# Optimization experiments

Hardware: AMD Instinct MI355X
Metric: run time of the kernel (lower is better)

The kernel has to match this reference:

```python
import jax, jax.numpy as jnp
import numpy as np

BETA = 0.9
ADAPT_RATE = 0.1


def _surrogate_spike(x):
    gate = jax.nn.sigmoid(5.0 * x)
    hard = (x > 0).astype(x.dtype)
    return jax.lax.stop_gradient(hard - gate) + gate


def setup_inputs() -> dict:
    key = jax.random.key(0)
    k1, k2, k3, k4, k5 = jax.random.split(key, 5)
    B, T, D, H = 64, 256, 512, 1024
    x = jax.random.normal(k1, (B, T, D), dtype=jnp.float32)
    # fc_in: Linear(D, H); fc_out: Linear(H, 1)
    W_in = jax.random.normal(k2, (H, D), dtype=jnp.float32) * (1.0 / np.sqrt(D))
    b_in = jax.random.normal(k3, (H,), dtype=jnp.float32) * 0.01
    W_out = jax.random.normal(k4, (1, H), dtype=jnp.float32) * (1.0 / np.sqrt(H))
    b_out = jax.random.normal(k5, (1,), dtype=jnp.float32) * 0.01
    return {"x": x, "W_in": W_in, "b_in": b_in, "W_out": W_out, "b_out": b_out}


def reference(x, W_in, b_in, W_out, b_out):
    B, T, D = x.shape
    H = W_in.shape[0]
    # batch fc_in over all timesteps outside the recurrence
    pre = jnp.einsum('btd,hd->bth', x, W_in) + b_in  # [B,T,H]

    def step(carry, p_t):
        mem, adapt = carry
        mem = BETA * mem + p_t - adapt
        spk = _surrogate_spike(mem)
        adapt = adapt + ADAPT_RATE * spk
        mem = mem - spk  # reset_mode == 'subtract'
        return (mem, adapt), spk

    init = (jnp.zeros((B, H), x.dtype), jnp.zeros((B, H), x.dtype))
    _, spks = jax.lax.scan(step, init, jnp.swapaxes(pre, 0, 1))  # spks: [T,B,H]

    # mean_t fc_out(spk_t) == fc_out(mean_t spk_t) since fc_out is affine
    spk_mean = spks.mean(axis=0)  # [B,H]
    return spk_mean @ W_out.T + b_out  # [B,1]
```

## Files before the change

### kernel.cpp

```cpp
#include <hip/hip_runtime.h>

constexpr int Bb = 64;
constexpr int Tt = 256;
constexpr int Dd = 512;
constexpr int Hh = 1024;
constexpr int Mm = Bb * Tt;

typedef _Float16 half8 __attribute__((ext_vector_type(8)));
typedef _Float16 half4v __attribute__((ext_vector_type(4)));
typedef float floatx16 __attribute__((ext_vector_type(16)));

#define GPTR(x) ((const __attribute__((address_space(1))) void*)(x))
#define LPTR(x) ((__attribute__((address_space(3))) void*)(x))

__global__ __launch_bounds__(256) void convert_t(const float* __restrict__ x,
                                                 const float* __restrict__ Win,
                                                 _Float16* __restrict__ xh,
                                                 _Float16* __restrict__ xl,
                                                 _Float16* __restrict__ wh,
                                                 _Float16* __restrict__ wl,
                                                 const float* __restrict__ bout,
                                                 float* __restrict__ out) {
    __shared__ _Float16 lh[64 * 72];
    __shared__ _Float16 ll[64 * 72];
    const int tid = threadIdx.x;
    const int k0 = blockIdx.x * 64;

    if (blockIdx.x == 0 && blockIdx.y == 0 && tid < Bb) out[tid] = bout[0];

    const float* src;
    _Float16 *dh, *dl;
    int nrows, m0;
    if (blockIdx.y < 256) {
        src = x; dh = xh; dl = xl; nrows = Mm; m0 = blockIdx.y * 64;
    } else {
        src = Win; dh = wh; dl = wl; nrows = Hh; m0 = (blockIdx.y - 256) * 64;
    }

#pragma unroll
    for (int i = 0; i < 4; ++i) {
        const int lin = tid + i * 256;
        const int row = lin >> 4;
        const int c4 = (lin & 15) * 4;
        const float4 v = *(const float4*)(src + (size_t)(m0 + row) * Dd + k0 + c4);
        const float va[4] = {v.x, v.y, v.z, v.w};
        half4v h, l;
#pragma unroll
        for (int q = 0; q < 4; ++q) {
            const _Float16 hi = (_Float16)va[q];
            h[q] = hi;
            l[q] = (_Float16)((va[q] - (float)hi) * 4096.0f);
        }
        *(half4v*)&lh[row * 72 + c4] = h;
        *(half4v*)&ll[row * 72 + c4] = l;
    }
    __syncthreads();
#pragma unroll
    for (int i = 0; i < 2; ++i) {
        const int lin = tid + i * 256;
        const int kc = lin >> 6;
        const int mm = lin & 63;
        const half8 h = *(const half8*)&lh[mm * 72 + kc * 8];
        const half8 l = *(const half8*)&ll[mm * 72 + kc * 8];
        const size_t g = (size_t)(k0 / 8 + kc) * nrows + m0 + mm;
        *(half8*)(dh + g * 8) = h;
        *(half8*)(dl + g * 8) = l;
    }
}

__global__ __launch_bounds__(256, 2) void gemm_fused(const _Float16* __restrict__ xh,
                                                     const _Float16* __restrict__ xl,
                                                     const _Float16* __restrict__ wh,
                                                     const _Float16* __restrict__ wl,
                                                     const float* __restrict__ bin,
                                                     const float* __restrict__ Wout,
                                                     float* __restrict__ out) {
    __shared__ _Float16 ldsA[2][2][8192];

    const int tid = threadIdx.x;
    const int id = blockIdx.x;
    const int j  = id & 7;
    const int q  = id >> 3;
    const int nt = q & 15;
    const int b  = (q >> 4) * 8 + j;
    const int m0 = b * Tt;
    const int n0 = nt * 64;

    const int lane = tid & 63;
    const int wave = tid >> 6;
    const int lr = lane & 31;
    const int lk = lane >> 5;

    floatx16 acc[2][2], accx[2][2];
#pragma unroll
    for (int mi = 0; mi < 2; ++mi)
#pragma unroll
        for (int ni = 0; ni < 2; ++ni)
#pragma unroll
            for (int r = 0; r < 16; ++r) { acc[mi][ni][r] = 0.0f; accx[mi][ni][r] = 0.0f; }

#define STAGE_A(buf, kc0)                                                            \
    do {                                                                             \
        _Pragma("unroll")                                                            \
        for (int i_ = 0; i_ < 4; ++i_) {                                             \
            const int c_ = tid + i_ * 256;                                           \
            const int kp_ = c_ >> 8;                                                 \
            const int row_ = c_ & 255;                                               \
            const size_t ga_ = ((size_t)((kc0) + kp_) * Mm + m0 + row_) * 8;         \
            __builtin_amdgcn_global_load_lds(GPTR(xh + ga_), LPTR(&ldsA[buf][0][c_ * 8]), 16, 0, 0); \
            __builtin_amdgcn_global_load_lds(GPTR(xl + ga_), LPTR(&ldsA[buf][1][c_ * 8]), 16, 0, 0); \
        }                                                                            \
    } while (0)

    const size_t bbase = (size_t)(n0 + lr) * 8;
    half8 bset[2][4];
#define LOAD_B(rot, hs)                                                              \
    do {                                                                             \
        const size_t off_ = (size_t)((hs) * 2 + lk) * (Hh * 8) + bbase;              \
        bset[rot][0] = *(const half8*)(wh + off_);                                   \
        bset[rot][1] = *(const half8*)(wh + off_ + 256);                             \
        bset[rot][2] = *(const half8*)(wl + off_);                                   \
        bset[rot][3] = *(const half8*)(wl + off_ + 256);                             \
    } while (0)

    STAGE_A(0, 0);
    LOAD_B(0, 0);

    for (int ss = 0; ss < 16; ++ss) {
        __syncthreads();
        if (ss < 15) STAGE_A((ss + 1) & 1, (ss + 1) * 4);
        const int cur = ss & 1;
#pragma unroll
        for (int s2 = 0; s2 < 2; ++s2) {
            const int hs = ss * 2 + s2;
            const int rot = hs & 1;
            if (hs < 31) LOAD_B(rot ^ 1, hs + 1);

            half8 ah[2], al[2];
#pragma unroll
            for (int mi = 0; mi < 2; ++mi) {
                const int ci = (s2 * 2 + lk) * 256 + wave * 64 + mi * 32 + lr;
                ah[mi] = *(const half8*)&ldsA[cur][0][ci * 8];
                al[mi] = *(const half8*)&ldsA[cur][1][ci * 8];
            }
#pragma unroll
            for (int mi = 0; mi < 2; ++mi)
#pragma unroll
                for (int ni = 0; ni < 2; ++ni) {
                    acc[mi][ni]  = __builtin_amdgcn_mfma_f32_32x32x16_f16(ah[mi], bset[rot][ni],     acc[mi][ni], 0, 0, 0);
                    accx[mi][ni] = __builtin_amdgcn_mfma_f32_32x32x16_f16(ah[mi], bset[rot][2 + ni], accx[mi][ni], 0, 0, 0);
                    accx[mi][ni] = __builtin_amdgcn_mfma_f32_32x32x16_f16(al[mi], bset[rot][ni],     accx[mi][ni], 0, 0, 0);
                }
        }
    }
#undef STAGE_A
#undef LOAD_B

    __syncthreads();
    float* scanbuf = (float*)ldsA;

#pragma unroll
    for (int p = 0; p < 2; ++p) {
        const float bv = bin[n0 + p * 32 + lr];
#pragma unroll
        for (int mi = 0; mi < 2; ++mi)
#pragma unroll
            for (int r = 0; r < 16; ++r) {
                const int row = (r & 3) + 8 * (r >> 2) + 4 * lk;
                const int t = wave * 64 + mi * 32 + row;
                scanbuf[p * 8192 + t * 32 + lr] =
                    acc[mi][p][r] + accx[mi][p][r] * (1.0f / 4096.0f) + bv;
            }
    }
    __syncthreads();

    if (wave == 0) {
        const float* sb = scanbuf + (lane >> 5) * 8192 + (lane & 31);
        float mem = 0.0f, adapt = 0.0f, cnt = 0.0f;
#pragma unroll 8
        for (int t = 0; t < Tt; ++t) {
            const float v = sb[t * 32];
            mem = 0.9f * mem + v - adapt;
            const float spk = (mem > 0.0f) ? 1.0f : 0.0f;
            adapt += 0.1f * spk;
            mem -= spk;
            cnt += spk;
        }
        float val = cnt * Wout[n0 + lane] * (1.0f / (float)Tt);
#pragma unroll
        for (int off = 32; off > 0; off >>= 1) val += __shfl_down(val, off, 64);
        if (lane == 0) atomicAdd(&out[b], val);
    }
}

#define BK 16
#define BMP 132
__global__ __launch_bounds__(256) void gemm_pre(const float* __restrict__ x,
                                                const float* __restrict__ Win,
                                                const float* __restrict__ bin,
                                                float* __restrict__ pre) {
    __shared__ float As[BK][BMP];
    __shared__ float Bs[BK][BMP];
    const int tid = threadIdx.x;
    const int m0 = blockIdx.y * 128;
    const int n0 = blockIdx.x * 128;
    const int tx = tid & 15;
    const int ty = tid >> 4;
    float acc[8][8];
#pragma unroll
    for (int i = 0; i < 8; ++i)
#pragma unroll
        for (int jj = 0; jj < 8; ++jj) acc[i][jj] = 0.0f;
    const float* Aptr = x + (size_t)m0 * Dd;
    const float* Bptr = Win + (size_t)n0 * Dd;
    for (int k0 = 0; k0 < Dd; k0 += BK) {
#pragma unroll
        for (int i = 0; i < 2; ++i) {
            const int lin = tid + i * 256;
            const int row = lin >> 2;
            const int kq = (lin & 3) << 2;
            const float4 av = *(const float4*)(Aptr + (size_t)row * Dd + k0 + kq);
            const float4 bv = *(const float4*)(Bptr + (size_t)row * Dd + k0 + kq);
            As[kq + 0][row] = av.x; As[kq + 1][row] = av.y;
            As[kq + 2][row] = av.z; As[kq + 3][row] = av.w;
            Bs[kq + 0][row] = bv.x; Bs[kq + 1][row] = bv.y;
            Bs[kq + 2][row] = bv.z; Bs[kq + 3][row] = bv.w;
        }
        __syncthreads();
#pragma unroll
        for (int kk = 0; kk < BK; ++kk) {
            const float4 a0 = *(const float4*)&As[kk][ty * 4];
            const float4 a1 = *(const float4*)&As[kk][ty * 4 + 64];
            const float4 b0 = *(const float4*)&Bs[kk][tx * 4];
            const float4 b1 = *(const float4*)&Bs[kk][tx * 4 + 64];
            const float a[8] = {a0.x, a0.y, a0.z, a0.w, a1.x, a1.y, a1.z, a1.w};
            const float b[8] = {b0.x, b0.y, b0.z, b0.w, b1.x, b1.y, b1.z, b1.w};
#pragma unroll
            for (int i = 0; i < 8; ++i)
#pragma unroll
                for (int jj = 0; jj < 8; ++jj) acc[i][jj] += a[i] * b[jj];
        }
        __syncthreads();
    }
#pragma unroll
    for (int i = 0; i < 8; ++i) {
        const int m = m0 + ((i < 4) ? (ty * 4 + i) : (64 + ty * 4 + i - 4));
#pragma unroll
        for (int half = 0; half < 2; ++half) {
            const int n = n0 + tx * 4 + half * 64;
            float4 v;
            v.x = acc[i][half * 4 + 0] + bin[n + 0];
            v.y = acc[i][half * 4 + 1] + bin[n + 1];
            v.z = acc[i][half * 4 + 2] + bin[n + 2];
            v.w = acc[i][half * 4 + 3] + bin[n + 3];
            *(float4*)(pre + (size_t)m * Hh + n) = v;
        }
    }
}

__global__ __launch_bounds__(64) void init_out(const float* __restrict__ bout,
                                               float* __restrict__ out) {
    out[threadIdx.x] = bout[0];
}

__global__ __launch_bounds__(64) void alif_scan(const float* __restrict__ pre,
                                                const float* __restrict__ Wout,
                                                float* __restrict__ out) {
    const int h = blockIdx.x * 64 + threadIdx.x;
    const int b = blockIdx.y;
    const float* p = pre + (size_t)b * Tt * Hh + h;

    float buf[32];
#pragma unroll
    for (int jj = 0; jj < 32; ++jj) buf[jj] = p[(size_t)jj * Hh];

    float mem = 0.0f, adapt = 0.0f, cnt = 0.0f;
    for (int t0 = 0; t0 < Tt; t0 += 32) {
        float cur[32];
#pragma unroll
        for (int jj = 0; jj < 32; ++jj) cur[jj] = buf[jj];
        if (t0 + 32 < Tt) {
#pragma unroll
            for (int jj = 0; jj < 32; ++jj) buf[jj] = p[(size_t)(t0 + 32 + jj) * Hh];
        }
#pragma unroll
        for (int jj = 0; jj < 32; ++jj) {
            mem = 0.9f * mem + cur[jj] - adapt;
            const float spk = (mem > 0.0f) ? 1.0f : 0.0f;
            adapt += 0.1f * spk;
            mem -= spk;
            cnt += spk;
        }
    }

    float val = cnt * Wout[h] * (1.0f / (float)Tt);
#pragma unroll
    for (int off = 32; off > 0; off >>= 1) val += __shfl_down(val, off, 64);
    if (threadIdx.x == 0) atomicAdd(&out[b], val);
}

extern "C" void kernel_launch(void* const* d_in, const int* in_sizes, int n_in,
                              void* d_out, int out_size, void* d_ws, size_t ws_size,
                              hipStream_t stream) {
    const float* x    = (const float*)d_in[0];
    const float* Win  = (const float*)d_in[1];
    const float* bin  = (const float*)d_in[2];
    const float* Wout = (const float*)d_in[3];
    const float* bout = (const float*)d_in[4];
    float* out = (float*)d_out;

    const size_t xh_bytes = (size_t)Mm * Dd * 2;
    const size_t wh_bytes = (size_t)Hh * Dd * 2;
    const size_t need = 2 * xh_bytes + 2 * wh_bytes + 4096;

    if (ws_size >= need) {
        char* base = (char*)d_ws;
        _Float16* xh = (_Float16*)base;
        _Float16* xl = (_Float16*)(base + xh_bytes);
        _Float16* wh = (_Float16*)(base + 2 * xh_bytes);
        _Float16* wl = (_Float16*)(base + 2 * xh_bytes + wh_bytes);

        convert_t<<<dim3(8, 272), 256, 0, stream>>>(x, Win, xh, xl, wh, wl, bout, out);

        gemm_fused<<<1024, 256, 0, stream>>>(xh, xl, wh, wl, bin, Wout, out);
    } else {
        float* pre = (float*)d_ws;
        init_out<<<1, 64, 0, stream>>>(bout, out);
        dim3 g1(Hh / 128, Mm / 128);
        gemm_pre<<<g1, 256, 0, stream>>>(x, Win, bin, pre);
        alif_scan<<<dim3(Hh / 64, Bb), 64, 0, stream>>>(pre, Wout, out);
    }
}
```

Baseline: 148.6 us.

## Widen fused GEMM tile to 128 columns with 8 waves; simplify convert kernel

The fused GEMM now uses 512-thread blocks where two wave groups share one staged A tile across 128 output columns. This halves how often x is reloaded from global memory and halves the grid. The scan epilogue runs in two phases through the shared LDS buffer, which adds a barrier, and the grid drops to 512 blocks. The convert kernel is rewritten without LDS: each thread converts 16 contiguous floats and writes the k-chunked fp16 hi/lo layout directly, removing a barrier and the shared-memory transpose.

```diff
diff --git a/kernel.cpp b/kernel.cpp
--- a/kernel.cpp
+++ b/kernel.cpp
@@ -7,7 +7,6 @@
 constexpr int Mm = Bb * Tt;
 
 typedef _Float16 half8 __attribute__((ext_vector_type(8)));
-typedef _Float16 half4v __attribute__((ext_vector_type(4)));
 typedef float floatx16 __attribute__((ext_vector_type(16)));
 
 #define GPTR(x) ((const __attribute__((address_space(1))) void*)(x))
@@ -21,54 +20,53 @@
                                                  _Float16* __restrict__ wl,
                                                  const float* __restrict__ bout,
                                                  float* __restrict__ out) {
-    __shared__ _Float16 lh[64 * 72];
-    __shared__ _Float16 ll[64 * 72];
     const int tid = threadIdx.x;
-    const int k0 = blockIdx.x * 64;
-
-    if (blockIdx.x == 0 && blockIdx.y == 0 && tid < Bb) out[tid] = bout[0];
+    if (blockIdx.x == 0 && tid < Bb) out[tid] = bout[0];
+
+    const int gw = (blockIdx.x * 256 + tid) >> 6;
+    const int lane = tid & 63;
 
     const float* src;
     _Float16 *dh, *dl;
-    int nrows, m0;
-    if (blockIdx.y < 256) {
-        src = x; dh = xh; dl = xl; nrows = Mm; m0 = blockIdx.y * 64;
+    int nrows, kcp, rg;
+    if (gw < 8192) {
+        src = x; dh = xh; dl = xl; nrows = Mm;
+        kcp = gw >> 8;
+        rg  = gw & 255;
     } else {
-        src = Win; dh = wh; dl = wl; nrows = Hh; m0 = (blockIdx.y - 256) * 64;
-    }
-
-#pragma unroll
-    for (int i = 0; i < 4; ++i) {
-        const int lin = tid + i * 256;
-        const int row = lin >> 4;
-        const int c4 = (lin & 15) * 4;
-        const float4 v = *(const float4*)(src + (size_t)(m0 + row) * Dd + k0 + c4);
-        const float va[4] = {v.x, v.y, v.z, v.w};
-        half4v h, l;
-#pragma unroll
-        for (int q = 0; q < 4; ++q) {
-            const _Float16 hi = (_Float16)va[q];
-            h[q] = hi;
-            l[q] = (_Float16)((va[q] - (float)hi) * 4096.0f);
-        }
-        *(half4v*)&lh[row * 72 + c4] = h;
-        *(half4v*)&ll[row * 72 + c4] = l;
-    }
-    __syncthreads();
-#pragma unroll
-    for (int i = 0; i < 2; ++i) {
-        const int lin = tid + i * 256;
-        const int kc = lin >> 6;
-        const int mm = lin & 63;
-        const half8 h = *(const half8*)&lh[mm * 72 + kc * 8];
-        const half8 l = *(const half8*)&ll[mm * 72 + kc * 8];
-        const size_t g = (size_t)(k0 / 8 + kc) * nrows + m0 + mm;
-        *(half8*)(dh + g * 8) = h;
-        *(half8*)(dl + g * 8) = l;
-    }
-}
-
-__global__ __launch_bounds__(256, 2) void gemm_fused(const _Float16* __restrict__ xh,
+        src = Win; dh = wh; dl = wl; nrows = Hh;
+        const int u = gw - 8192;
+        kcp = u >> 4;
+        rg  = u & 15;
+    }
+    const int row = rg * 64 + lane;
+    const float* p = src + (size_t)row * Dd + kcp * 16;
+
+    const float4 v0 = ((const float4*)p)[0];
+    const float4 v1 = ((const float4*)p)[1];
+    const float4 v2 = ((const float4*)p)[2];
+    const float4 v3 = ((const float4*)p)[3];
+    const float va[16] = {v0.x, v0.y, v0.z, v0.w, v1.x, v1.y, v1.z, v1.w,
+                          v2.x, v2.y, v2.z, v2.w, v3.x, v3.y, v3.z, v3.w};
+    half8 h[2], l[2];
+#pragma unroll
+    for (int c = 0; c < 2; ++c)
+#pragma unroll
+        for (int q = 0; q < 8; ++q) {
+            const float v = va[c * 8 + q];
+            const _Float16 hi = (_Float16)v;
+            h[c][q] = hi;
+            l[c][q] = (_Float16)((v - (float)hi) * 4096.0f);
+        }
+#pragma unroll
+    for (int c = 0; c < 2; ++c) {
+        const size_t g = (size_t)(kcp * 2 + c) * nrows + row;
+        *(half8*)(dh + g * 8) = h[c];
+        *(half8*)(dl + g * 8) = l[c];
+    }
+}
+
+__global__ __launch_bounds__(512, 2) void gemm_fused(const _Float16* __restrict__ xh,
                                                      const _Float16* __restrict__ xl,
                                                      const _Float16* __restrict__ wh,
                                                      const _Float16* __restrict__ wl,
@@ -80,14 +78,16 @@
     const int tid = threadIdx.x;
     const int id = blockIdx.x;
     const int j  = id & 7;
-    const int q  = id >> 3;
-    const int nt = q & 15;
-    const int b  = (q >> 4) * 8 + j;
+    const int s  = id >> 3;
+    const int nt = s & 7;
+    const int b  = (s >> 3) * 8 + j;
     const int m0 = b * Tt;
-    const int n0 = nt * 64;
+    const int n0 = nt * 128;
 
     const int lane = tid & 63;
     const int wave = tid >> 6;
+    const int wm = wave & 3;
+    const int wn = wave >> 2;
     const int lr = lane & 31;
     const int lk = lane >> 5;
 
@@ -102,8 +102,8 @@
 #define STAGE_A(buf, kc0)                                                            \
     do {                                                                             \
         _Pragma("unroll")                                                            \
-        for (int i_ = 0; i_ < 4; ++i_) {                                             \
-            const int c_ = tid + i_ * 256;                                           \
+        for (int i_ = 0; i_ < 2; ++i_) {                                             \
+            const int c_ = tid + i_ * 512;                                           \
             const int kp_ = c_ >> 8;                                                 \
             const int row_ = c_ & 255;                                               \
             const size_t ga_ = ((size_t)((kc0) + kp_) * Mm + m0 + row_) * 8;         \
@@ -112,7 +112,7 @@
         }                                                                            \
     } while (0)
 
-    const size_t bbase = (size_t)(n0 + lr) * 8;
+    const size_t bbase = (size_t)(n0 + wn * 64 + lr) * 8;
     half8 bset[2][4];
 #define LOAD_B(rot, hs)                                                              \
     do {                                                                             \
@@ -139,7 +139,7 @@
             half8 ah[2], al[2];
 #pragma unroll
             for (int mi = 0; mi < 2; ++mi) {
-                const int ci = (s2 * 2 + lk) * 256 + wave * 64 + mi * 32 + lr;
+                const int ci = (s2 * 2 + lk) * 256 + wm * 64 + mi * 32 + lr;
                 ah[mi] = *(const half8*)&ldsA[cur][0][ci * 8];
                 al[mi] = *(const half8*)&ldsA[cur][1][ci * 8];
             }
@@ -156,40 +156,45 @@
 #undef STAGE_A
 #undef LOAD_B
 
+    float* scanbuf = (float*)ldsA;
+
     __syncthreads();
-    float* scanbuf = (float*)ldsA;
-
 #pragma unroll
     for (int p = 0; p < 2; ++p) {
-        const float bv = bin[n0 + p * 32 + lr];
-#pragma unroll
-        for (int mi = 0; mi < 2; ++mi)
-#pragma unroll
-            for (int r = 0; r < 16; ++r) {
-                const int row = (r & 3) + 8 * (r >> 2) + 4 * lk;
-                const int t = wave * 64 + mi * 32 + row;
-                scanbuf[p * 8192 + t * 32 + lr] =
-                    acc[mi][p][r] + accx[mi][p][r] * (1.0f / 4096.0f) + bv;
+        if (wn == p) {
+#pragma unroll
+            for (int ni = 0; ni < 2; ++ni) {
+                const float bv = bin[n0 + p * 64 + ni * 32 + lr];
+#pragma unroll
+                for (int mi = 0; mi < 2; ++mi)
+#pragma unroll
+                    for (int r = 0; r < 16; ++r) {
+                        const int row = (r & 3) + 8 * (r >> 2) + 4 * lk;
+                        const int t = wm * 64 + mi * 32 + row;
+                        scanbuf[ni * 8192 + t * 32 + lr] =
+                            acc[mi][ni][r] + accx[mi][ni][r] * (1.0f / 4096.0f) + bv;
+                    }
             }
-    }
-    __syncthreads();
-
-    if (wave == 0) {
-        const float* sb = scanbuf + (lane >> 5) * 8192 + (lane & 31);
-        float mem = 0.0f, adapt = 0.0f, cnt = 0.0f;
+        }
+        __syncthreads();
+        if (wave == p * 4) {
+            const float* sb = scanbuf + (lane >> 5) * 8192 + (lane & 31);
+            float mem = 0.0f, adapt = 0.0f, cnt = 0.0f;
 #pragma unroll 8
-        for (int t = 0; t < Tt; ++t) {
-            const float v = sb[t * 32];
-            mem = 0.9f * mem + v - adapt;
-            const float spk = (mem > 0.0f) ? 1.0f : 0.0f;
-            adapt += 0.1f * spk;
-            mem -= spk;
-            cnt += spk;
-        }
-        float val = cnt * Wout[n0 + lane] * (1.0f / (float)Tt);
-#pragma unroll
-        for (int off = 32; off > 0; off >>= 1) val += __shfl_down(val, off, 64);
-        if (lane == 0) atomicAdd(&out[b], val);
+            for (int t = 0; t < Tt; ++t) {
+                const float v = sb[t * 32];
+                mem = 0.9f * mem + v - adapt;
+                const float spk = (mem > 0.0f) ? 1.0f : 0.0f;
+                adapt += 0.1f * spk;
+                mem -= spk;
+                cnt += spk;
+            }
+            float val = cnt * Wout[n0 + p * 64 + lane] * (1.0f / (float)Tt);
+#pragma unroll
+            for (int off = 32; off > 0; off >>= 1) val += __shfl_down(val, off, 64);
+            if (lane == 0) atomicAdd(&out[b], val);
+        }
+        if (p == 0) __syncthreads();
     }
 }
 
@@ -320,9 +325,9 @@
         _Float16* wh = (_Float16*)(base + 2 * xh_bytes);
         _Float16* wl = (_Float16*)(base + 2 * xh_bytes + wh_bytes);
 
-        convert_t<<<dim3(8, 272), 256, 0, stream>>>(x, Win, xh, xl, wh, wl, bout, out);
-
-        gemm_fused<<<1024, 256, 0, stream>>>(xh, xl, wh, wl, bin, Wout, out);
+        convert_t<<<2176, 256, 0, stream>>>(x, Win, xh, xl, wh, wl, bout, out);
+
+        gemm_fused<<<512, 512, 0, stream>>>(xh, xl, wh, wl, bin, Wout, out);
     } else {
         float* pre = (float*)d_ws;
         init_out<<<1, 64, 0, stream>>>(bout, out);
```

Result: slower. 159.6 us (+7.4%).

## Swap operand staging: stream W tiles through LDS, load x directly to registers

Applied to the files above, without the earlier changes.

The GEMM mainloop now stages the small W_in tile (64 columns) into double-buffered LDS via global_load_lds and loads each wave's private x rows straight from global memory into registers. Before, it staged the large 256-row x tile through LDS and read W from global. Since each wave owns distinct M rows, A needs no LDS sharing, while B is shared across all four waves. This cuts LDS traffic and the per-stage staging volume, and stages 8 K-chunks per sync so there are half as many barriers. In exchange, more register pressure comes from the direct A loads, and global latency for x is exposed per wave.

```diff
diff --git a/kernel.cpp b/kernel.cpp
--- a/kernel.cpp
+++ b/kernel.cpp
@@ -75,7 +75,8 @@
                                                      const float* __restrict__ bin,
                                                      const float* __restrict__ Wout,
                                                      float* __restrict__ out) {
-    __shared__ _Float16 ldsA[2][2][8192];
+    __shared__ float ldsS[16384];
+    _Float16* ldsB = (_Float16*)ldsS;
 
     const int tid = threadIdx.x;
     const int id = blockIdx.x;
@@ -99,65 +100,65 @@
 #pragma unroll
             for (int r = 0; r < 16; ++r) { acc[mi][ni][r] = 0.0f; accx[mi][ni][r] = 0.0f; }
 
-#define STAGE_A(buf, kc0)                                                            \
+#define STAGE_B(buf, SS)                                                             \
     do {                                                                             \
         _Pragma("unroll")                                                            \
-        for (int i_ = 0; i_ < 4; ++i_) {                                             \
+        for (int i_ = 0; i_ < 2; ++i_) {                                             \
             const int c_ = tid + i_ * 256;                                           \
-            const int kp_ = c_ >> 8;                                                 \
-            const int row_ = c_ & 255;                                               \
-            const size_t ga_ = ((size_t)((kc0) + kp_) * Mm + m0 + row_) * 8;         \
-            __builtin_amdgcn_global_load_lds(GPTR(xh + ga_), LPTR(&ldsA[buf][0][c_ * 8]), 16, 0, 0); \
-            __builtin_amdgcn_global_load_lds(GPTR(xl + ga_), LPTR(&ldsA[buf][1][c_ * 8]), 16, 0, 0); \
+            const int kc_ = c_ >> 6;                                                 \
+            const int col_ = c_ & 63;                                                \
+            const size_t g_ = ((size_t)((SS) * 8 + kc_) * Hh + n0 + col_) * 8;       \
+            __builtin_amdgcn_global_load_lds(GPTR(wh + g_), LPTR(&ldsB[((buf) * 2 + 0) * 4096 + c_ * 8]), 16, 0, 0); \
+            __builtin_amdgcn_global_load_lds(GPTR(wl + g_), LPTR(&ldsB[((buf) * 2 + 1) * 4096 + c_ * 8]), 16, 0, 0); \
         }                                                                            \
     } while (0)
 
-    const size_t bbase = (size_t)(n0 + lr) * 8;
-    half8 bset[2][4];
-#define LOAD_B(rot, hs)                                                              \
+    const size_t arow0 = (size_t)(m0 + wave * 64 + lr);
+    half8 aset[2][4];
+#define LOAD_A(rot, hs)                                                              \
     do {                                                                             \
-        const size_t off_ = (size_t)((hs) * 2 + lk) * (Hh * 8) + bbase;              \
-        bset[rot][0] = *(const half8*)(wh + off_);                                   \
-        bset[rot][1] = *(const half8*)(wh + off_ + 256);                             \
-        bset[rot][2] = *(const half8*)(wl + off_);                                   \
-        bset[rot][3] = *(const half8*)(wl + off_ + 256);                             \
+        const size_t kA = (size_t)((hs) * 2 + lk) * Mm;                              \
+        aset[rot][0] = *(const half8*)(xh + (kA + arow0) * 8);                       \
+        aset[rot][1] = *(const half8*)(xh + (kA + arow0 + 32) * 8);                  \
+        aset[rot][2] = *(const half8*)(xl + (kA + arow0) * 8);                       \
+        aset[rot][3] = *(const half8*)(xl + (kA + arow0 + 32) * 8);                  \
     } while (0)
 
-    STAGE_A(0, 0);
-    LOAD_B(0, 0);
-
-    for (int ss = 0; ss < 16; ++ss) {
+    STAGE_B(0, 0);
+    LOAD_A(0, 0);
+
+    for (int SS = 0; SS < 8; ++SS) {
         __syncthreads();
-        if (ss < 15) STAGE_A((ss + 1) & 1, (ss + 1) * 4);
-        const int cur = ss & 1;
-#pragma unroll
-        for (int s2 = 0; s2 < 2; ++s2) {
-            const int hs = ss * 2 + s2;
+        if (SS < 7) STAGE_B((SS + 1) & 1, SS + 1);
+        const int cur = SS & 1;
+#pragma unroll
+        for (int qq = 0; qq < 4; ++qq) {
+            const int hs = SS * 4 + qq;
             const int rot = hs & 1;
-            if (hs < 31) LOAD_B(rot ^ 1, hs + 1);
-
-            half8 ah[2], al[2];
-#pragma unroll
-            for (int mi = 0; mi < 2; ++mi) {
-                const int ci = (s2 * 2 + lk) * 256 + wave * 64 + mi * 32 + lr;
-                ah[mi] = *(const half8*)&ldsA[cur][0][ci * 8];
-                al[mi] = *(const half8*)&ldsA[cur][1][ci * 8];
+            if (hs < 31) LOAD_A(rot ^ 1, hs + 1);
+
+            half8 bh[2], bl[2];
+#pragma unroll
+            for (int ni = 0; ni < 2; ++ni) {
+                const int ci = (qq * 2 + lk) * 64 + ni * 32 + lr;
+                bh[ni] = *(const half8*)&ldsB[(cur * 2 + 0) * 4096 + ci * 8];
+                bl[ni] = *(const half8*)&ldsB[(cur * 2 + 1) * 4096 + ci * 8];
             }
 #pragma unroll
             for (int mi = 0; mi < 2; ++mi)
 #pragma unroll
                 for (int ni = 0; ni < 2; ++ni) {
-                    acc[mi][ni]  = __builtin_amdgcn_mfma_f32_32x32x16_f16(ah[mi], bset[rot][ni],     acc[mi][ni], 0, 0, 0);
-                    accx[mi][ni] = __builtin_amdgcn_mfma_f32_32x32x16_f16(ah[mi], bset[rot][2 + ni], accx[mi][ni], 0, 0, 0);
-                    accx[mi][ni] = __builtin_amdgcn_mfma_f32_32x32x16_f16(al[mi], bset[rot][ni],     accx[mi][ni], 0, 0, 0);
+                    acc[mi][ni]  = __builtin_amdgcn_mfma_f32_32x32x16_f16(aset[rot][mi],     bh[ni], acc[mi][ni], 0, 0, 0);
+                    accx[mi][ni] = __builtin_amdgcn_mfma_f32_32x32x16_f16(aset[rot][mi],     bl[ni], accx[mi][ni], 0, 0, 0);
+                    accx[mi][ni] = __builtin_amdgcn_mfma_f32_32x32x16_f16(aset[rot][2 + mi], bh[ni], accx[mi][ni], 0, 0, 0);
                 }
         }
     }
-#undef STAGE_A
-#undef LOAD_B
+#undef STAGE_B
+#undef LOAD_A
 
     __syncthreads();
-    float* scanbuf = (float*)ldsA;
+    float* scanbuf = ldsS;
 
 #pragma unroll
     for (int p = 0; p < 2; ++p) {
```

Measured after the change: 144.7 us (median of 2 runs). 1.03x faster.
